# Optimization experiments

Measured on AMD Instinct MI355X. Metric: run time of the kernel, lower is better.

Reference implementation:

```python
import jax, jax.numpy as jnp
import numpy as np

B, SQ, SKV, D = 4, 2048, 2048, 768
H, HD = 12, 16  # num_heads, reduced head_dim (64 / reduce_factor 4)
DR = H * HD     # 192 reduced width


def setup_inputs() -> dict:
    key = jax.random.key(0)
    ks = jax.random.split(key, 6)
    s = 0.02
    return {
        "hidden_states": jax.random.normal(ks[0], (B, SQ, D), jnp.float32),
        "encoder_hidden_states": jax.random.normal(ks[1], (B, SKV, D), jnp.float32),
        "Wq": jax.random.normal(ks[2], (D, DR), jnp.float32) * s,
        "bq": jnp.zeros((DR,), jnp.float32),
        "Wkv": jax.random.normal(ks[3], (D, 2 * DR), jnp.float32) * s,
        "bkv": jnp.zeros((2 * DR,), jnp.float32),
        "Wp": jax.random.normal(ks[4], (DR, D), jnp.float32) * s,
        "bp": jnp.zeros((D,), jnp.float32),
    }


def _split_heads(x):
    # [B, S, DR] -> [B, H, S, HD]
    b, s, _ = x.shape
    return x.reshape(b, s, H, HD).transpose(0, 2, 1, 3)


def reference(hidden_states, encoder_hidden_states, Wq, bq, Wkv, bkv, Wp, bp):
    # Conv1D projections (x @ W + b)
    q = hidden_states @ Wq + bq                       # [B, SQ, 192]
    kv = encoder_hidden_states @ Wkv + bkv            # [B, SKV, 384]
    k, v = kv[..., :DR], kv[..., DR:]
    q = _split_heads(q)                               # [B, H, SQ, HD]
    k = _split_heads(k)                               # [B, H, SKV, HD]
    v = _split_heads(v)                               # [B, H, SKV, HD]
    scale = jnp.asarray(HD, q.dtype) ** 0.5
    scores = jnp.einsum('bhqd,bhkd->bhqk', q, k) / scale
    attn = jax.nn.softmax(scores, axis=-1)            # dropout is identity in eval
    out = jnp.einsum('bhqk,bhkd->bhqd', attn, v)      # [B, H, SQ, HD]
    out = out.transpose(0, 2, 1, 3).reshape(hidden_states.shape[0], -1, DR)
    out = out @ Wp + bp                               # [B, SQ, 768]
    return out
```

## Files before the change

kernel.cpp:

```cpp
#include <hip/hip_runtime.h>
#include <hip/hip_bf16.h>
#include <math.h>

#define NB 4
#define NSQ 2048
#define NSKV 2048
#define ND 768
#define NH 12
#define NHD 16
#define NDR 192
#define M_TOT (NB * NSQ)

typedef __attribute__((ext_vector_type(8)))  short          bf16x8;
typedef __attribute__((ext_vector_type(16))) float          f32x16;
typedef __attribute__((ext_vector_type(8)))  unsigned short u16x8;

__device__ __forceinline__ unsigned short bfbits(float x) {
  __hip_bfloat16 h = __float2bfloat16(x);
  unsigned short u; __builtin_memcpy(&u, &h, 2); return u;
}
__device__ __forceinline__ float bf2f(unsigned short u) {
  unsigned int v = ((unsigned int)u) << 16; float f; __builtin_memcpy(&f, &v, 4); return f;
}
__device__ __forceinline__ unsigned int pk2t(float a, float b) {
  unsigned int ua, ub;
  __builtin_memcpy(&ua, &a, 4); __builtin_memcpy(&ub, &b, 4);
#if __has_builtin(__builtin_amdgcn_perm)
  return __builtin_amdgcn_perm(ub, ua, 0x07060302);
#else
  return (ua >> 16) | (ub & 0xffff0000u);
#endif
}
__device__ __forceinline__ float exp2_raw(float x) {
#if __has_builtin(__builtin_amdgcn_exp2f)
  return __builtin_amdgcn_exp2f(x);
#else
  float r; asm("v_exp_f32 %0, %1" : "=v"(r) : "v"(x)); return r;
#endif
}
__device__ __forceinline__ void g2l16(const void* g, void* l) {
  __builtin_amdgcn_global_load_lds(
      (const __attribute__((address_space(1))) void*)g,
      (__attribute__((address_space(3))) void*)l, 16, 0, 0);
}

#define QSCALE 0.36067376022224085f
#define LDSBUF 16384

__global__ __launch_bounds__(256) void prep(
    const float* __restrict__ Wq, const float* __restrict__ Wkv,
    const float* __restrict__ Wp,
    unsigned short* __restrict__ WSq, unsigned short* __restrict__ WSkv,
    unsigned short* __restrict__ WSp) {
  int bid = blockIdx.x;
  const float* W; unsigned short* out; int Nn, KBLK, bx, by;
  if (bid < 72)        { W = Wq;  out = WSq;  Nn = 192; KBLK = 24; bx = bid % 24;        by = bid / 24; }
  else if (bid < 216)  { int b = bid - 72;  W = Wkv; out = WSkv; Nn = 384; KBLK = 24; bx = b % 24; by = b / 24; }
  else                 { int b = bid - 216; W = Wp;  out = WSp;  Nn = 768; KBLK = 6;  bx = b % 6;  by = b / 6;  }

  __shared__ float tile[32][65];
  int k0 = bx * 32, n0 = by * 64;
  int t = threadIdx.x;
  int kr = t >> 3, c0 = (t & 7) * 8;
  const float* src = W + (size_t)(k0 + kr) * Nn + n0 + c0;
  float4 f0 = *reinterpret_cast<const float4*>(src);
  float4 f1 = *reinterpret_cast<const float4*>(src + 4);
  tile[kr][c0+0] = f0.x; tile[kr][c0+1] = f0.y; tile[kr][c0+2] = f0.z; tile[kr][c0+3] = f0.w;
  tile[kr][c0+4] = f1.x; tile[kr][c0+5] = f1.y; tile[kr][c0+6] = f1.z; tile[kr][c0+7] = f1.w;
  __syncthreads();
  int n = t >> 2, cq0 = (t & 3) * 2;
  int ng = n0 + n, sw = ng & 7;
  unsigned short* dst = out + ((size_t)ng * KBLK + bx) * 64;
  #pragma unroll
  for (int q = 0; q < 2; ++q) {
    int cc = cq0 + q;
    u16x8 v;
    #pragma unroll
    for (int i = 0; i < 8; ++i) {
      float x = tile[(cc & 3) * 8 + i][n];
      unsigned short h = bfbits(x);
      v[i] = (cc < 4) ? h : bfbits(x - bf2f(h));
    }
    *reinterpret_cast<u16x8*>(dst + (cc ^ sw) * 8) = v;
  }
}

__device__ __forceinline__ void core_compute(
    const unsigned short* const (&ard)[4], const unsigned short* const (&wrd)[12],
    int off, f32x16 (&acc)[3]) {
  #pragma unroll
  for (int kk = 0; kk < 2; ++kk) {
    bf16x8 ah = *reinterpret_cast<const bf16x8*>(ard[kk*2+0] + off);
    bf16x8 al = *reinterpret_cast<const bf16x8*>(ard[kk*2+1] + off);
    #pragma unroll
    for (int nr = 0; nr < 3; ++nr) {
      bf16x8 wh = *reinterpret_cast<const bf16x8*>(wrd[(nr*2+kk)*2+0] + off);
      bf16x8 wl = *reinterpret_cast<const bf16x8*>(wrd[(nr*2+kk)*2+1] + off);
      acc[nr] = __builtin_amdgcn_mfma_f32_32x32x16_bf16(ah, wh, acc[nr], 0, 0, 0);
      acc[nr] = __builtin_amdgcn_mfma_f32_32x32x16_bf16(ah, wl, acc[nr], 0, 0, 0);
      acc[nr] = __builtin_amdgcn_mfma_f32_32x32x16_bf16(al, wh, acc[nr], 0, 0, 0);
    }
  }
}

__device__ __forceinline__ void gemm_core(
    const unsigned short* __restrict__ As,
    const unsigned short* __restrict__ Ws,
    const float* __restrict__ bias,
    int KBLK, unsigned short* lds, f32x16 (&acc)[3]) {
  const int tid = threadIdx.x;
  const int wv = tid >> 6, lane = tid & 63;
  const int l31 = lane & 31, hi8 = lane >> 5;
  const int wm = wv >> 1, wn = wv & 1;

  unsigned short* Ab = lds;
  unsigned short* Wb = lds + 64 * 64;

  const int r8 = lane >> 3, c8 = lane & 7;
  const size_t rowu = (size_t)KBLK * 64;

  const unsigned short* srcA0 = As + (size_t)((0*4 + wv)*8 + r8) * rowu + c8*8;
  const unsigned short* srcA1 = As + (size_t)((1*4 + wv)*8 + r8) * rowu + c8*8;
  const unsigned short* srcW[6];
  #pragma unroll
  for (int j = 0; j < 6; ++j)
    srcW[j] = Ws + (size_t)((j*4 + wv)*8 + r8) * rowu + c8*8;

  unsigned short* dA0 = Ab + ((0*4 + wv)*64 + lane) * 8;
  unsigned short* dA1 = Ab + ((1*4 + wv)*64 + lane) * 8;
  unsigned short* dW[6];
  #pragma unroll
  for (int j = 0; j < 6; ++j)
    dW[j] = Wb + ((j*4 + wv)*64 + lane) * 8;

  const int ra = wm*32 + l31;
  const unsigned short* ard[4];
  #pragma unroll
  for (int kk = 0; kk < 2; ++kk) {
    ard[kk*2+0] = Ab + ra*64 + (((kk*2 + hi8)     ^ (ra & 7)) * 8);
    ard[kk*2+1] = Ab + ra*64 + (((4 + kk*2 + hi8) ^ (ra & 7)) * 8);
  }
  const unsigned short* wrd[12];
  #pragma unroll
  for (int nr = 0; nr < 3; ++nr) {
    int rw = wn*96 + nr*32 + l31;
    #pragma unroll
    for (int kk = 0; kk < 2; ++kk) {
      wrd[(nr*2+kk)*2+0] = Wb + rw*64 + (((kk*2 + hi8)     ^ (rw & 7)) * 8);
      wrd[(nr*2+kk)*2+1] = Wb + rw*64 + (((4 + kk*2 + hi8) ^ (rw & 7)) * 8);
    }
  }

  #pragma unroll
  for (int nr = 0; nr < 3; ++nr) {
    float bv = bias[wn*96 + nr*32 + l31];
    #pragma unroll
    for (int r = 0; r < 16; ++r) acc[nr][r] = bv;
  }

  g2l16(srcA0, dA0); srcA0 += 64;
  g2l16(srcA1, dA1); srcA1 += 64;
  #pragma unroll
  for (int j = 0; j < 6; ++j) { g2l16(srcW[j], dW[j]); srcW[j] += 64; }
  __syncthreads();

  for (int kb = 0; kb < KBLK; kb += 2) {
    if (kb + 1 < KBLK) {
      g2l16(srcA0, dA0 + LDSBUF); srcA0 += 64;
      g2l16(srcA1, dA1 + LDSBUF); srcA1 += 64;
      #pragma unroll
      for (int j = 0; j < 6; ++j) { g2l16(srcW[j], dW[j] + LDSBUF); srcW[j] += 64; }
    }
    core_compute(ard, wrd, 0, acc);
    __syncthreads();
    if (kb + 2 < KBLK) {
      g2l16(srcA0, dA0); srcA0 += 64;
      g2l16(srcA1, dA1); srcA1 += 64;
      #pragma unroll
      for (int j = 0; j < 6; ++j) { g2l16(srcW[j], dW[j]); srcW[j] += 64; }
    }
    core_compute(ard, wrd, LDSBUF, acc);
    __syncthreads();
  }
}

#define QHALF 10240
__global__ __launch_bounds__(384) void gemm_qkv(
    const float* __restrict__ A1, const float* __restrict__ A2,
    const unsigned short* __restrict__ WSq, const unsigned short* __restrict__ WSkv,
    const float* __restrict__ bq, const float* __restrict__ bkv,
    unsigned short* __restrict__ Qbf, unsigned short* __restrict__ Kbf,
    unsigned short* __restrict__ VTbf) {
  __shared__ unsigned short lds[2 * QHALF];
  const int bid = blockIdx.x;
  const float* Afp; const unsigned short* Ws; const float* bias;
  int m0, mode, ntile;
  if (bid < 256) {
    mode = 0; ntile = (bid >> 7) * 96;
    Afp = A1; Ws = WSq + (size_t)ntile * (24*64); bias = bq + ntile;
    m0 = (bid & 127) * 64;
  } else {
    int b2 = bid - 256;
    int sub = b2 >> 7;
    m0 = (b2 & 127) * 64;
    Afp = A2;
    if (sub < 2) { mode = 1; ntile = sub * 96;
                   Ws = WSkv + (size_t)ntile * (24*64); bias = bkv + ntile; }
    else         { mode = 2; ntile = (sub - 2) * 96;
                   Ws = WSkv + (size_t)(192 + ntile) * (24*64); bias = bkv + 192 + ntile; }
  }
  Afp += (size_t)m0 * ND;

  const int tid = threadIdx.x;
  const int wv = tid >> 6, lane = tid & 63;
  const int l31 = lane & 31, hi8 = lane >> 5;
  const int wm = wv & 1, wn = wv >> 1;

  unsigned short* Ab = lds;
  unsigned short* Wb = lds + 64*64;

  const int ar = tid >> 2, cq = tid & 3;
  const bool doA = (tid < 256);
  const float* srcA = Afp + (size_t)(doA ? ar : 0) * ND + cq*8;
  unsigned short* dAh = Ab + (doA ? ar : 0)*64 + ((cq       ^ (ar & 7)) * 8);
  unsigned short* dAl = Ab + (doA ? ar : 0)*64 + (((cq + 4) ^ (ar & 7)) * 8);

  const int wch0 = tid, wch1 = tid + 384;
  const unsigned short* srcW0 = Ws + (size_t)(wch0 >> 3) * (24*64) + (wch0 & 7) * 8;
  const unsigned short* srcW1 = Ws + (size_t)(wch1 >> 3) * (24*64) + (wch1 & 7) * 8;
  unsigned short* dW0 = Wb + wch0 * 8;
  unsigned short* dW1 = Wb + wch1 * 8;

  const int ra = wm*32 + l31;
  const int rw = wn*32 + l31;
  const unsigned short* ard[4];
  const unsigned short* wrd[4];
  #pragma unroll
  for (int kk = 0; kk < 2; ++kk) {
    ard[kk*2+0] = Ab + ra*64 + (((kk*2 + hi8)     ^ (ra & 7)) * 8);
    ard[kk*2+1] = Ab + ra*64 + (((4 + kk*2 + hi8) ^ (ra & 7)) * 8);
    wrd[kk*2+0] = Wb + rw*64 + (((kk*2 + hi8)     ^ (rw & 7)) * 8);
    wrd[kk*2+1] = Wb + rw*64 + (((4 + kk*2 + hi8) ^ (rw & 7)) * 8);
  }

  f32x16 acc;
  {
    float bv = bias[wn*32 + l31];
    #pragma unroll
    for (int r = 0; r < 16; ++r) acc[r] = bv;
  }

  {
    g2l16(srcW0, dW0); srcW0 += 64;
    g2l16(srcW1, dW1); srcW1 += 64;
    if (doA) {
      float4 f0 = *reinterpret_cast<const float4*>(srcA);
      float4 f1 = *reinterpret_cast<const float4*>(srcA + 4);
      float x[8] = {f0.x, f0.y, f0.z, f0.w, f1.x, f1.y, f1.z, f1.w};
      u16x8 hv, lv;
      #pragma unroll
      for (int i = 0; i < 8; ++i) {
        unsigned short h = bfbits(x[i]);
        hv[i] = h; lv[i] = bfbits(x[i] - bf2f(h));
      }
      *reinterpret_cast<u16x8*>(dAh) = hv;
      *reinterpret_cast<u16x8*>(dAl) = lv;
    }
    srcA += 32;
  }
  __syncthreads();

  #define QKV_COMPUTE(off)                                                     \
    {                                                                          \
      _Pragma("unroll")                                                        \
      for (int kk = 0; kk < 2; ++kk) {                                         \
        bf16x8 ah = *reinterpret_cast<const bf16x8*>(ard[kk*2+0] + (off));     \
        bf16x8 al = *reinterpret_cast<const bf16x8*>(ard[kk*2+1] + (off));     \
        bf16x8 wh = *reinterpret_cast<const bf16x8*>(wrd[kk*2+0] + (off));     \
        bf16x8 wl = *reinterpret_cast<const bf16x8*>(wrd[kk*2+1] + (off));     \
        acc = __builtin_amdgcn_mfma_f32_32x32x16_bf16(ah, wh, acc, 0, 0, 0);   \
        acc = __builtin_amdgcn_mfma_f32_32x32x16_bf16(ah, wl, acc, 0, 0, 0);   \
        acc = __builtin_amdgcn_mfma_f32_32x32x16_bf16(al, wh, acc, 0, 0, 0);   \
      }                                                                        \
    }

  for (int kb = 0; kb < 24; kb += 2) {
    float4 f0, f1;
    g2l16(srcW0, dW0 + QHALF); srcW0 += 64;
    g2l16(srcW1, dW1 + QHALF); srcW1 += 64;
    if (doA) {
      f0 = *reinterpret_cast<const float4*>(srcA);
      f1 = *reinterpret_cast<const float4*>(srcA + 4);
    }
    srcA += 32;
    QKV_COMPUTE(0)
    if (doA) {
      float x[8] = {f0.x, f0.y, f0.z, f0.w, f1.x, f1.y, f1.z, f1.w};
      u16x8 hv, lv;
      #pragma unroll
      for (int i = 0; i < 8; ++i) {
        unsigned short h = bfbits(x[i]);
        hv[i] = h; lv[i] = bfbits(x[i] - bf2f(h));
      }
      *reinterpret_cast<u16x8*>(dAh + QHALF) = hv;
      *reinterpret_cast<u16x8*>(dAl + QHALF) = lv;
    }
    __syncthreads();
    bool has2 = (kb + 2 < 24);
    if (has2) {
      g2l16(srcW0, dW0); srcW0 += 64;
      g2l16(srcW1, dW1); srcW1 += 64;
      if (doA) {
        f0 = *reinterpret_cast<const float4*>(srcA);
        f1 = *reinterpret_cast<const float4*>(srcA + 4);
      }
      srcA += 32;
    }
    QKV_COMPUTE(QHALF)
    if (has2 && doA) {
      float x[8] = {f0.x, f0.y, f0.z, f0.w, f1.x, f1.y, f1.z, f1.w};
      u16x8 hv, lv;
      #pragma unroll
      for (int i = 0; i < 8; ++i) {
        unsigned short h = bfbits(x[i]);
        hv[i] = h; lv[i] = bfbits(x[i] - bf2f(h));
      }
      *reinterpret_cast<u16x8*>(dAh) = hv;
      *reinterpret_cast<u16x8*>(dAl) = lv;
    }
    __syncthreads();
  }
  #undef QKV_COMPUTE

  if (mode == 2) {
    unsigned short (*tile)[65] = reinterpret_cast<unsigned short(*)[65]>(lds);
    #pragma unroll
    for (int r = 0; r < 16; ++r) {
      int key_l = wm*32 + (r & 3) + 8*(r >> 2) + 4*hi8;
      tile[wn*32 + l31][key_l] = bfbits(acc[r]);
    }
    __syncthreads();
    int b = m0 >> 11, key0 = m0 & 2047;
    #pragma unroll
    for (int j = 0; j < 2; ++j) {
      int flat = j * 384 + tid;
      int row = flat >> 3;
      int ck = flat & 7;
      int vcol = ntile + row;
      int h = vcol >> 4, d = vcol & 15;
      u16x8 v;
      #pragma unroll
      for (int jj = 0; jj < 8; ++jj) v[jj] = tile[row][ck*8 + jj];
      *reinterpret_cast<u16x8*>(
          &VTbf[(((size_t)(b*NH + h)*256 + (key0 >> 3) + ck)*16 + d)*8]) = v;
    }
    return;
  }

  unsigned short* outp = (mode == 0) ? Qbf : Kbf;
  const float scale = (mode == 0) ? QSCALE : 1.0f;
  {
    int col = ntile + wn*32 + l31;
    int h = col >> 4, d = col & 15;
    #pragma unroll
    for (int r = 0; r < 16; ++r) {
      int mg = m0 + wm*32 + (r & 3) + 8*(r >> 2) + 4*hi8;
      int b = mg >> 11, q = mg & 2047;
      outp[(((size_t)b*NH + h)*NSQ + q)*16 + d] = bfbits(acc[r] * scale);
    }
  }
}

__device__ __forceinline__ void attn_tile32x2(
    bf16x8 qfA, bf16x8 qfB, bf16x8 kf, bf16x8 vf0, bf16x8 vf1,
    int hi8, const f32x16& zeroc, f32x16& accA, f32x16& accB) {
  f32x16 sA = __builtin_amdgcn_mfma_f32_32x32x16_bf16(kf, qfA, zeroc, 0, 0, 0);
  f32x16 sB = __builtin_amdgcn_mfma_f32_32x32x16_bf16(kf, qfB, zeroc, 0, 0, 0);

  float pA[16], pB[16];
  #pragma unroll
  for (int r = 0; r < 16; ++r) { pA[r] = exp2_raw(sA[r]); pB[r] = exp2_raw(sB[r]); }

  unsigned int wA[8], wB[8];
  #pragma unroll
  for (int t8 = 0; t8 < 8; ++t8) {
    wA[t8] = pk2t(pA[2*t8], pA[2*t8+1]);
    wB[t8] = pk2t(pB[2*t8], pB[2*t8+1]);
  }

  unsigned int tA0 = hi8 ? wA[0] : wA[2], tA1 = hi8 ? wA[1] : wA[3];
  unsigned int tA2 = hi8 ? wA[4] : wA[6], tA3 = hi8 ? wA[5] : wA[7];
  unsigned int tB0 = hi8 ? wB[0] : wB[2], tB1 = hi8 ? wB[1] : wB[3];
  unsigned int tB2 = hi8 ? wB[4] : wB[6], tB3 = hi8 ? wB[5] : wB[7];
  unsigned int rA0 = (unsigned int)__shfl_xor((int)tA0, 32);
  unsigned int rA1 = (unsigned int)__shfl_xor((int)tA1, 32);
  unsigned int rA2 = (unsigned int)__shfl_xor((int)tA2, 32);
  unsigned int rA3 = (unsigned int)__shfl_xor((int)tA3, 32);
  unsigned int rB0 = (unsigned int)__shfl_xor((int)tB0, 32);
  unsigned int rB1 = (unsigned int)__shfl_xor((int)tB1, 32);
  unsigned int rB2 = (unsigned int)__shfl_xor((int)tB2, 32);
  unsigned int rB3 = (unsigned int)__shfl_xor((int)tB3, 32);

  union { bf16x8 v; unsigned int u[4]; } pa0A, pa1A, pa0B, pa1B;
  pa0A.u[0] = hi8 ? rA0 : wA[0];  pa0A.u[1] = hi8 ? rA1 : wA[1];
  pa0A.u[2] = hi8 ? wA[2] : rA0;  pa0A.u[3] = hi8 ? wA[3] : rA1;
  pa1A.u[0] = hi8 ? rA2 : wA[4];  pa1A.u[1] = hi8 ? rA3 : wA[5];
  pa1A.u[2] = hi8 ? wA[6] : rA2;  pa1A.u[3] = hi8 ? wA[7] : rA3;
  pa0B.u[0] = hi8 ? rB0 : wB[0];  pa0B.u[1] = hi8 ? rB1 : wB[1];
  pa0B.u[2] = hi8 ? wB[2] : rB0;  pa0B.u[3] = hi8 ? wB[3] : rB1;
  pa1B.u[0] = hi8 ? rB2 : wB[4];  pa1B.u[1] = hi8 ? rB3 : wB[5];
  pa1B.u[2] = hi8 ? wB[6] : rB2;  pa1B.u[3] = hi8 ? wB[7] : rB3;

  __builtin_amdgcn_s_setprio(1);
  accA = __builtin_amdgcn_mfma_f32_32x32x16_bf16(vf0, pa0A.v, accA, 0, 0, 0);
  accB = __builtin_amdgcn_mfma_f32_32x32x16_bf16(vf0, pa0B.v, accB, 0, 0, 0);
  accA = __builtin_amdgcn_mfma_f32_32x32x16_bf16(vf1, pa1A.v, accA, 0, 0, 0);
  accB = __builtin_amdgcn_mfma_f32_32x32x16_bf16(vf1, pa1B.v, accB, 0, 0, 0);
  __builtin_amdgcn_s_setprio(0);
}

__global__ __launch_bounds__(256, 3) void attn_bf16(
    const unsigned short* __restrict__ Qbf, const unsigned short* __restrict__ Kbf,
    const unsigned short* __restrict__ VT, unsigned short* __restrict__ AOS) {
  __shared__ float comb[2][4][64][9];
  const int tid = threadIdx.x;
  const int wave = tid >> 6, lane = tid & 63;
  const int l31 = lane & 31, hi8 = lane >> 5;
  const int bid = blockIdx.x;
  const int bh = bid % 48;
  const int qt = bid / 48;

  const unsigned short* qp = &Qbf[((size_t)bh*NSQ + qt*64 + l31)*16 + hi8*8];
  bf16x8 qfA = *reinterpret_cast<const bf16x8*>(qp);
  bf16x8 qfB = *reinterpret_cast<const bf16x8*>(qp + 32*16);
  const unsigned short* kbase = Kbf + (size_t)bh * NSKV * 16;

  const short fillv = (l31 == 16) ? (short)0x3F80 : (short)0;
  bf16x8 vfill;
  #pragma unroll
  for (int j = 0; j < 8; ++j) vfill[j] = fillv;

  f32x16 accA, accB;
  #pragma unroll
  for (int r = 0; r < 16; ++r) { accA[r] = 0.f; accB[r] = 0.f; }
  const f32x16 zeroc = accA;

  const int kstart = wave * (NSKV / 4);
  const unsigned short* kp = &kbase[(size_t)(kstart + l31)*16 + hi8*8];
  const unsigned short* vwave = VT + ((((size_t)bh*256 + (kstart >> 3) + hi8)*16 + l31) * 8);

  bf16x8 k0, v00, v10;
  bf16x8 k1, v01, v11;

  k0  = *reinterpret_cast<const bf16x8*>(kp);
  v00 = vfill; v10 = vfill;
  if (l31 < 16) {
    v00 = *reinterpret_cast<const bf16x8*>(vwave);
    v10 = *reinterpret_cast<const bf16x8*>(vwave + 256);
  }

  for (int kt = 0; kt < 512; kt += 64) {
    {
      k1 = *reinterpret_cast<const bf16x8*>(kp + (size_t)(kt + 32) * 16);
      v01 = vfill; v11 = vfill;
      if (l31 < 16) {
        const unsigned short* vq = vwave + (size_t)(kt + 32) * 16;
        v01 = *reinterpret_cast<const bf16x8*>(vq);
        v11 = *reinterpret_cast<const bf16x8*>(vq + 256);
      }
    }
    attn_tile32x2(qfA, qfB, k0, v00, v10, hi8, zeroc, accA, accB);
    if (kt + 64 < 512) {
      k0 = *reinterpret_cast<const bf16x8*>(kp + (size_t)(kt + 64) * 16);
      v00 = vfill; v10 = vfill;
      if (l31 < 16) {
        const unsigned short* vq = vwave + (size_t)(kt + 64) * 16;
        v00 = *reinterpret_cast<const bf16x8*>(vq);
        v10 = *reinterpret_cast<const bf16x8*>(vq + 256);
      }
    }
    attn_tile32x2(qfA, qfB, k1, v01, v11, hi8, zeroc, accA, accB);
  }

  {
    float* cbA = &comb[0][wave][lane][0];
    float* cbB = &comb[1][wave][lane][0];
    #pragma unroll
    for (int r = 0; r < 9; ++r) { cbA[r] = accA[r]; cbB[r] = accB[r]; }
  }
  __syncthreads();

  if (wave < 2) {
    const int g = wave;
    float A[9];
    #pragma unroll
    for (int r = 0; r < 9; ++r)
      A[r] = ((comb[g][0][lane][r] + comb[g][1][lane][r]) +
              (comb[g][2][lane][r] + comb[g][3][lane][r]));
    float L = A[8] + __shfl_xor(A[8], 32);
    float inv = 1.f / L;

    unsigned short oh[8], ol[8];
    #pragma unroll
    for (int r = 0; r < 8; ++r) {
      float o = A[r] * inv;
      oh[r] = bfbits(o);
      ol[r] = bfbits(o - bf2f(oh[r]));
    }
    int b = bh / NH, h = bh % NH;
    int q = qt*64 + g*32 + l31;
    int mrow = b * NSQ + q;
    unsigned short* rowp = AOS + (size_t)mrow * (6 * 64);
    int sw = mrow & 7;
    int kblk = h >> 1;
    int cA = (h & 1) * 2;
    unsigned short* p0;
    p0 = rowp + ((kblk*8 + ((cA + 0) ^ sw)) * 8) + 4*hi8;
    reinterpret_cast<unsigned int*>(p0)[0] = (unsigned)oh[0] | ((unsigned)oh[1] << 16);
    reinterpret_cast<unsigned int*>(p0)[1] = (unsigned)oh[2] | ((unsigned)oh[3] << 16);
    p0 = rowp + ((kblk*8 + ((cA + 1) ^ sw)) * 8) + 4*hi8;
    reinterpret_cast<unsigned int*>(p0)[0] = (unsigned)oh[4] | ((unsigned)oh[5] << 16);
    reinterpret_cast<unsigned int*>(p0)[1] = (unsigned)oh[6] | ((unsigned)oh[7] << 16);
    p0 = rowp + ((kblk*8 + ((cA + 4) ^ sw)) * 8) + 4*hi8;
    reinterpret_cast<unsigned int*>(p0)[0] = (unsigned)ol[0] | ((unsigned)ol[1] << 16);
    reinterpret_cast<unsigned int*>(p0)[1] = (unsigned)ol[2] | ((unsigned)ol[3] << 16);
    p0 = rowp + ((kblk*8 + ((cA + 5) ^ sw)) * 8) + 4*hi8;
    reinterpret_cast<unsigned int*>(p0)[0] = (unsigned)ol[4] | ((unsigned)ol[5] << 16);
    reinterpret_cast<unsigned int*>(p0)[1] = (unsigned)ol[6] | ((unsigned)ol[7] << 16);
  }
}

__global__ __launch_bounds__(256) void gemm_out_k(
    const unsigned short* __restrict__ AOS, const unsigned short* __restrict__ WSp,
    const float* __restrict__ bp, float* __restrict__ out) {
  __shared__ unsigned short lds[2 * LDSBUF];
  const int bid = blockIdx.x;
  const int KBLK = NDR / 32;
  int m0 = (bid & 127) * 64;
  int n0 = (bid >> 7) * 192;
  const unsigned short* As = AOS + (size_t)m0 * KBLK * 64;
  const unsigned short* Ws = WSp + (size_t)n0 * KBLK * 64;
  f32x16 acc[3];
  gemm_core(As, Ws, bp + n0, KBLK, lds, acc);

  const int tid = threadIdx.x;
  const int wv = tid >> 6, lane = tid & 63;
  const int l31 = lane & 31, hi8 = lane >> 5;
  const int wm = wv >> 1, wn = wv & 1;
  #pragma unroll
  for (int nr = 0; nr < 3; ++nr) {
    int n = n0 + wn*96 + nr*32 + l31;
    #pragma unroll
    for (int r = 0; r < 16; ++r) {
      int mg = m0 + wm*32 + (r & 3) + 8*(r >> 2) + 4*hi8;
      out[(size_t)mg * ND + n] = acc[nr][r];
    }
  }
}

extern "C" void kernel_launch(void* const* d_in, const int* in_sizes, int n_in,
                              void* d_out, int out_size, void* d_ws, size_t ws_size,
                              hipStream_t stream) {
  const float* hs  = (const float*)d_in[0];
  const float* ehs = (const float*)d_in[1];
  const float* Wq  = (const float*)d_in[2];
  const float* bq  = (const float*)d_in[3];
  const float* Wkv = (const float*)d_in[4];
  const float* bkv = (const float*)d_in[5];
  const float* Wp  = (const float*)d_in[6];
  const float* bp  = (const float*)d_in[7];
  float* out = (float*)d_out;

  char* w = (char*)d_ws;
  unsigned short* AOS = (unsigned short*)w;
  char* w2 = w + (size_t)M_TOT * 6 * 64 * 2;
  unsigned short* WSq  = (unsigned short*)w2;
  unsigned short* WSkv = (unsigned short*)(w2 + 589824);
  unsigned short* WSp  = (unsigned short*)(w2 + 589824 + 1179648);
  char* w3 = w2 + 589824 + 1179648 + 589824;
  unsigned short* Qbf  = (unsigned short*)w3;
  unsigned short* Kbf  = Qbf + (size_t)M_TOT * NDR;
  unsigned short* VTbf = Kbf + (size_t)M_TOT * NDR;

  prep<<<dim3(72 + 144 + 72), dim3(256), 0, stream>>>(
      Wq, Wkv, Wp, WSq, WSkv, WSp);
  gemm_qkv<<<dim3(768), dim3(384), 0, stream>>>(hs, ehs, WSq, WSkv, bq, bkv, Qbf, Kbf, VTbf);
  attn_bf16<<<dim3(NB * NH * 32), dim3(256), 0, stream>>>(Qbf, Kbf, VTbf, AOS);
  gemm_out_k<<<dim3(512), dim3(256), 0, stream>>>(AOS, WSp, bp, out);
}
```

Before: 83.16 us.

## Retile output projection GEMM into 64x96 tiles with six waves

The output projection GEMM moves from 512 blocks of 4 waves, each computing a 64x192 tile with three accumulators per wave, to 1024 blocks of 6 waves, each computing a 64x96 tile with one 32x32 accumulator per wave. The load mapping is redistributed across 384 threads, with a predicated second A chunk, and the shared gemm_core helper is removed. The goal is more parallelism and better CU fill for a short K=192 GEMM. In exchange, each wave does less MFMA work per LDS load, which lowers arithmetic intensity and loads the A tile more often overall.

```diff
diff --git a/kernel.cpp b/kernel.cpp
--- a/kernel.cpp
+++ b/kernel.cpp
@@ -45,7 +45,6 @@
 }
 
 #define QSCALE 0.36067376022224085f
-#define LDSBUF 16384
 
 __global__ __launch_bounds__(256) void prep(
     const float* __restrict__ Wq, const float* __restrict__ Wkv,
@@ -82,105 +81,6 @@
       v[i] = (cc < 4) ? h : bfbits(x - bf2f(h));
     }
     *reinterpret_cast<u16x8*>(dst + (cc ^ sw) * 8) = v;
-  }
-}
-
-__device__ __forceinline__ void core_compute(
-    const unsigned short* const (&ard)[4], const unsigned short* const (&wrd)[12],
-    int off, f32x16 (&acc)[3]) {
-  #pragma unroll
-  for (int kk = 0; kk < 2; ++kk) {
-    bf16x8 ah = *reinterpret_cast<const bf16x8*>(ard[kk*2+0] + off);
-    bf16x8 al = *reinterpret_cast<const bf16x8*>(ard[kk*2+1] + off);
-    #pragma unroll
-    for (int nr = 0; nr < 3; ++nr) {
-      bf16x8 wh = *reinterpret_cast<const bf16x8*>(wrd[(nr*2+kk)*2+0] + off);
-      bf16x8 wl = *reinterpret_cast<const bf16x8*>(wrd[(nr*2+kk)*2+1] + off);
-      acc[nr] = __builtin_amdgcn_mfma_f32_32x32x16_bf16(ah, wh, acc[nr], 0, 0, 0);
-      acc[nr] = __builtin_amdgcn_mfma_f32_32x32x16_bf16(ah, wl, acc[nr], 0, 0, 0);
-      acc[nr] = __builtin_amdgcn_mfma_f32_32x32x16_bf16(al, wh, acc[nr], 0, 0, 0);
-    }
-  }
-}
-
-__device__ __forceinline__ void gemm_core(
-    const unsigned short* __restrict__ As,
-    const unsigned short* __restrict__ Ws,
-    const float* __restrict__ bias,
-    int KBLK, unsigned short* lds, f32x16 (&acc)[3]) {
-  const int tid = threadIdx.x;
-  const int wv = tid >> 6, lane = tid & 63;
-  const int l31 = lane & 31, hi8 = lane >> 5;
-  const int wm = wv >> 1, wn = wv & 1;
-
-  unsigned short* Ab = lds;
-  unsigned short* Wb = lds + 64 * 64;
-
-  const int r8 = lane >> 3, c8 = lane & 7;
-  const size_t rowu = (size_t)KBLK * 64;
-
-  const unsigned short* srcA0 = As + (size_t)((0*4 + wv)*8 + r8) * rowu + c8*8;
-  const unsigned short* srcA1 = As + (size_t)((1*4 + wv)*8 + r8) * rowu + c8*8;
-  const unsigned short* srcW[6];
-  #pragma unroll
-  for (int j = 0; j < 6; ++j)
-    srcW[j] = Ws + (size_t)((j*4 + wv)*8 + r8) * rowu + c8*8;
-
-  unsigned short* dA0 = Ab + ((0*4 + wv)*64 + lane) * 8;
-  unsigned short* dA1 = Ab + ((1*4 + wv)*64 + lane) * 8;
-  unsigned short* dW[6];
-  #pragma unroll
-  for (int j = 0; j < 6; ++j)
-    dW[j] = Wb + ((j*4 + wv)*64 + lane) * 8;
-
-  const int ra = wm*32 + l31;
-  const unsigned short* ard[4];
-  #pragma unroll
-  for (int kk = 0; kk < 2; ++kk) {
-    ard[kk*2+0] = Ab + ra*64 + (((kk*2 + hi8)     ^ (ra & 7)) * 8);
-    ard[kk*2+1] = Ab + ra*64 + (((4 + kk*2 + hi8) ^ (ra & 7)) * 8);
-  }
-  const unsigned short* wrd[12];
-  #pragma unroll
-  for (int nr = 0; nr < 3; ++nr) {
-    int rw = wn*96 + nr*32 + l31;
-    #pragma unroll
-    for (int kk = 0; kk < 2; ++kk) {
-      wrd[(nr*2+kk)*2+0] = Wb + rw*64 + (((kk*2 + hi8)     ^ (rw & 7)) * 8);
-      wrd[(nr*2+kk)*2+1] = Wb + rw*64 + (((4 + kk*2 + hi8) ^ (rw & 7)) * 8);
-    }
-  }
-
-  #pragma unroll
-  for (int nr = 0; nr < 3; ++nr) {
-    float bv = bias[wn*96 + nr*32 + l31];
-    #pragma unroll
-    for (int r = 0; r < 16; ++r) acc[nr][r] = bv;
-  }
-
-  g2l16(srcA0, dA0); srcA0 += 64;
-  g2l16(srcA1, dA1); srcA1 += 64;
-  #pragma unroll
-  for (int j = 0; j < 6; ++j) { g2l16(srcW[j], dW[j]); srcW[j] += 64; }
-  __syncthreads();
-
-  for (int kb = 0; kb < KBLK; kb += 2) {
-    if (kb + 1 < KBLK) {
-      g2l16(srcA0, dA0 + LDSBUF); srcA0 += 64;
-      g2l16(srcA1, dA1 + LDSBUF); srcA1 += 64;
-      #pragma unroll
-      for (int j = 0; j < 6; ++j) { g2l16(srcW[j], dW[j] + LDSBUF); srcW[j] += 64; }
-    }
-    core_compute(ard, wrd, 0, acc);
-    __syncthreads();
-    if (kb + 2 < KBLK) {
-      g2l16(srcA0, dA0); srcA0 += 64;
-      g2l16(srcA1, dA1); srcA1 += 64;
-      #pragma unroll
-      for (int j = 0; j < 6; ++j) { g2l16(srcW[j], dW[j]); srcW[j] += 64; }
-    }
-    core_compute(ard, wrd, LDSBUF, acc);
-    __syncthreads();
   }
 }
 
@@ -530,30 +430,104 @@
   }
 }
 
-__global__ __launch_bounds__(256) void gemm_out_k(
+__global__ __launch_bounds__(384) void gemm_out_k(
     const unsigned short* __restrict__ AOS, const unsigned short* __restrict__ WSp,
     const float* __restrict__ bp, float* __restrict__ out) {
-  __shared__ unsigned short lds[2 * LDSBUF];
+  __shared__ unsigned short lds[2 * QHALF];
   const int bid = blockIdx.x;
-  const int KBLK = NDR / 32;
-  int m0 = (bid & 127) * 64;
-  int n0 = (bid >> 7) * 192;
-  const unsigned short* As = AOS + (size_t)m0 * KBLK * 64;
-  const unsigned short* Ws = WSp + (size_t)n0 * KBLK * 64;
-  f32x16 acc[3];
-  gemm_core(As, Ws, bp + n0, KBLK, lds, acc);
+  const int m0 = (bid & 127) * 64;
+  const int n0 = (bid >> 7) * 96;
+
+  const unsigned short* As = AOS + (size_t)m0 * (6*64);
+  const unsigned short* Ws = WSp + (size_t)n0 * (6*64);
 
   const int tid = threadIdx.x;
   const int wv = tid >> 6, lane = tid & 63;
   const int l31 = lane & 31, hi8 = lane >> 5;
-  const int wm = wv >> 1, wn = wv & 1;
-  #pragma unroll
-  for (int nr = 0; nr < 3; ++nr) {
-    int n = n0 + wn*96 + nr*32 + l31;
+  const int wm = wv & 1, wn = wv >> 1;
+
+  unsigned short* Ab = lds;
+  unsigned short* Wb = lds + 64*64;
+
+  const bool doA2 = (tid < 128);
+  const int ach1 = tid + 384;
+  const unsigned short* srcA0 = As + (size_t)(tid >> 3) * (6*64) + (tid & 7) * 8;
+  const unsigned short* srcA1 = As + (size_t)(ach1 >> 3) * (6*64) + (ach1 & 7) * 8;
+  unsigned short* dA0 = Ab + tid * 8;
+  unsigned short* dA1 = Ab + ach1 * 8;
+
+  const int wch1 = tid + 384;
+  const unsigned short* srcW0 = Ws + (size_t)(tid >> 3) * (6*64) + (tid & 7) * 8;
+  const unsigned short* srcW1 = Ws + (size_t)(wch1 >> 3) * (6*64) + (wch1 & 7) * 8;
+  unsigned short* dW0 = Wb + tid * 8;
+  unsigned short* dW1 = Wb + wch1 * 8;
+
+  const int ra = wm*32 + l31;
+  const int rw = wn*32 + l31;
+  const unsigned short* ard[4];
+  const unsigned short* wrd[4];
+  #pragma unroll
+  for (int kk = 0; kk < 2; ++kk) {
+    ard[kk*2+0] = Ab + ra*64 + (((kk*2 + hi8)     ^ (ra & 7)) * 8);
+    ard[kk*2+1] = Ab + ra*64 + (((4 + kk*2 + hi8) ^ (ra & 7)) * 8);
+    wrd[kk*2+0] = Wb + rw*64 + (((kk*2 + hi8)     ^ (rw & 7)) * 8);
+    wrd[kk*2+1] = Wb + rw*64 + (((4 + kk*2 + hi8) ^ (rw & 7)) * 8);
+  }
+
+  f32x16 acc;
+  {
+    float bv = bp[n0 + wn*32 + l31];
+    #pragma unroll
+    for (int r = 0; r < 16; ++r) acc[r] = bv;
+  }
+
+  g2l16(srcA0, dA0); srcA0 += 64;
+  g2l16(srcW0, dW0); srcW0 += 64;
+  g2l16(srcW1, dW1); srcW1 += 64;
+  if (doA2) { g2l16(srcA1, dA1); }
+  srcA1 += 64;
+  __syncthreads();
+
+  #define OUT_COMPUTE(off)                                                     \
+    {                                                                          \
+      _Pragma("unroll")                                                        \
+      for (int kk = 0; kk < 2; ++kk) {                                         \
+        bf16x8 ah = *reinterpret_cast<const bf16x8*>(ard[kk*2+0] + (off));     \
+        bf16x8 al = *reinterpret_cast<const bf16x8*>(ard[kk*2+1] + (off));     \
+        bf16x8 wh = *reinterpret_cast<const bf16x8*>(wrd[kk*2+0] + (off));     \
+        bf16x8 wl = *reinterpret_cast<const bf16x8*>(wrd[kk*2+1] + (off));     \
+        acc = __builtin_amdgcn_mfma_f32_32x32x16_bf16(ah, wh, acc, 0, 0, 0);   \
+        acc = __builtin_amdgcn_mfma_f32_32x32x16_bf16(ah, wl, acc, 0, 0, 0);   \
+        acc = __builtin_amdgcn_mfma_f32_32x32x16_bf16(al, wh, acc, 0, 0, 0);   \
+      }                                                                        \
+    }
+
+  for (int kb = 0; kb < 6; kb += 2) {
+    g2l16(srcA0, dA0 + QHALF); srcA0 += 64;
+    g2l16(srcW0, dW0 + QHALF); srcW0 += 64;
+    g2l16(srcW1, dW1 + QHALF); srcW1 += 64;
+    if (doA2) { g2l16(srcA1, dA1 + QHALF); }
+    srcA1 += 64;
+    OUT_COMPUTE(0)
+    __syncthreads();
+    if (kb + 2 < 6) {
+      g2l16(srcA0, dA0); srcA0 += 64;
+      g2l16(srcW0, dW0); srcW0 += 64;
+      g2l16(srcW1, dW1); srcW1 += 64;
+      if (doA2) { g2l16(srcA1, dA1); }
+      srcA1 += 64;
+    }
+    OUT_COMPUTE(QHALF)
+    __syncthreads();
+  }
+  #undef OUT_COMPUTE
+
+  {
+    int n = n0 + wn*32 + l31;
     #pragma unroll
     for (int r = 0; r < 16; ++r) {
       int mg = m0 + wm*32 + (r & 3) + 8*(r >> 2) + 4*hi8;
-      out[(size_t)mg * ND + n] = acc[nr][r];
+      out[(size_t)mg * ND + n] = acc[r];
     }
   }
 }
@@ -586,5 +560,5 @@
       Wq, Wkv, Wp, WSq, WSkv, WSp);
   gemm_qkv<<<dim3(768), dim3(384), 0, stream>>>(hs, ehs, WSq, WSkv, bq, bkv, Qbf, Kbf, VTbf);
   attn_bf16<<<dim3(NB * NH * 32), dim3(256), 0, stream>>>(Qbf, Kbf, VTbf, AOS);
-  gemm_out_k<<<dim3(512), dim3(256), 0, stream>>>(AOS, WSp, bp, out);
-}
+  gemm_out_k<<<dim3(1024), dim3(384), 0, stream>>>(AOS, WSp, bp, out);
+}
```

Result: slower. 86.06 us (+3.5%).
